# Performance work log

Hardware: AMD Instinct MI355X
Metric: run time of the kernel (lower is better)

## Reference

```python
import jax, jax.numpy as jnp
import numpy as np

B, S, D, H = 2, 2048, 1024, 16
DK = D // H

def setup_inputs() -> dict:
    key = jax.random.key(0)
    ks = jax.random.split(key, 5)
    scale = 1.0 / np.sqrt(D)
    return {
        "query": jax.random.normal(ks[0], (B, S, D), dtype=jnp.float32),
        "mask": jnp.ones((B, S, S), dtype=jnp.int32),
        "Wq": jax.random.normal(ks[1], (D, D), dtype=jnp.float32) * scale,
        "bq": jnp.zeros((D,), dtype=jnp.float32),
        "Wk": jax.random.normal(ks[2], (D, D), dtype=jnp.float32) * scale,
        "bk": jnp.zeros((D,), dtype=jnp.float32),
        "Wv": jax.random.normal(ks[3], (D, D), dtype=jnp.float32) * scale,
        "bv": jnp.zeros((D,), dtype=jnp.float32),
        "Wo": jax.random.normal(ks[4], (D, D), dtype=jnp.float32) * scale,
        "bo": jnp.zeros((D,), dtype=jnp.float32),
    }

def reference(query, mask, Wq, bq, Wk, bk, Wv, bv, Wo, bo):
    # self-attention: key = value = query (torch Linear: x @ W.T + b)
    b, s, d = query.shape
    def proj(x, W, bias):
        y = jnp.einsum('bsd,ed->bse', x, W) + bias
        return y.reshape(b, s, H, DK).transpose(0, 2, 1, 3)  # [B,H,S,DK]
    q = proj(query, Wq, bq)
    k = proj(query, Wk, bk)
    v = proj(query, Wv, bv)
    scores = jnp.einsum('bhqd,bhkd->bhqk', q, k) / jnp.sqrt(jnp.float32(DK))
    m = mask[:, None, :, :]  # [B,1,S,S] (torch unsqueeze(1) for 3D mask)
    scores = jnp.where(m == 0, jnp.float32(-1e9), scores)
    w = jax.nn.softmax(scores, axis=-1)  # dropout: eval mode -> identity
    o = jnp.einsum('bhqk,bhkd->bhqd', w, v)
    o = o.transpose(0, 2, 1, 3).reshape(b, s, d)
    return jnp.einsum('bsd,ed->bse', o, Wo) + bo
```

## Files before the change

### kernel.cpp

```cpp
#include <hip/hip_runtime.h>


typedef _Float16 f16x8 __attribute__((ext_vector_type(8)));
typedef _Float16 f16x4 __attribute__((ext_vector_type(4)));
typedef float    f32x4 __attribute__((ext_vector_type(4)));
typedef float    f32x16 __attribute__((ext_vector_type(16)));
typedef int      i32x4 __attribute__((ext_vector_type(4)));

#define MFMA32(a, b, c) __builtin_amdgcn_mfma_f32_32x32x16_f16(a, b, c, 0, 0, 0)
#define MFMA16(a, b, c) __builtin_amdgcn_mfma_f32_16x16x32_f16(a, b, c, 0, 0, 0)

__device__ __forceinline__ void gld16(const void* g, void* l) {
    __builtin_amdgcn_global_load_lds(
        (const __attribute__((address_space(1))) void*)g,
        (__attribute__((address_space(3))) void*)l, 16, 0, 0);
}

__device__ __forceinline__ void conv1k(const float* __restrict__ in,
                                       _Float16* __restrict__ out, int base) {
    const int i = base + threadIdx.x * 4;
    float4 v = *(const float4*)(in + i);
    f16x4 o;
    o.x = (_Float16)v.x; o.y = (_Float16)v.y; o.z = (_Float16)v.z; o.w = (_Float16)v.w;
    *(f16x4*)(out + i) = o;
}

__global__ void k_pre(const float* __restrict__ X, const float* __restrict__ Wq,
                      const float* __restrict__ Wk, const float* __restrict__ Wv,
                      const float* __restrict__ Wo,
                      _Float16* __restrict__ Xh, _Float16* __restrict__ Wqh,
                      _Float16* __restrict__ Wkh, _Float16* __restrict__ Wvh,
                      _Float16* __restrict__ Woh,
                      const int* __restrict__ mask, int* __restrict__ flag) {
    const int bid = blockIdx.x;
    if (bid < 4096)      conv1k(X,  Xh,  bid * 1024);
    else if (bid < 5120) conv1k(Wq, Wqh, (bid - 4096) * 1024);
    else if (bid < 6144) conv1k(Wk, Wkh, (bid - 5120) * 1024);
    else if (bid < 7168) conv1k(Wv, Wvh, (bid - 6144) * 1024);
    else if (bid < 8192) conv1k(Wo, Woh, (bid - 7168) * 1024);
    else {
        const int i = (bid - 8192) * 1024 + threadIdx.x * 4;
        int4 v = *(const int4*)(mask + i);
        if ((v.x == 0) | (v.y == 0) | (v.z == 0) | (v.w == 0)) atomicOr(flag, 1);
    }
}

__global__ __launch_bounds__(256, 3) void k_qkv(
    const _Float16* __restrict__ X,
    const _Float16* __restrict__ Wqh, const _Float16* __restrict__ Wkh,
    const _Float16* __restrict__ Wvh,
    const float* __restrict__ bq, const float* __restrict__ bk,
    const float* __restrict__ bv,
    _Float16* __restrict__ Qo, _Float16* __restrict__ Ko, _Float16* __restrict__ Vo)
{
    __shared__ _Float16 SH[128 * 136];
    _Float16* As = SH;
    _Float16* Bs = SH + 128 * 64;
    const int tid = threadIdx.x;
    const int lane = tid & 63, wv = tid >> 6;
    const int wrow = wv >> 1, wcol = wv & 1;
    const int l5 = lane & 31, half = lane >> 5;
    const int which = blockIdx.x >> 3;
    const _Float16* W   = which == 0 ? Wqh : which == 1 ? Wkh : Wvh;
    const float*   bias = which == 0 ? bq  : which == 1 ? bk  : bv;
    const int n0 = (blockIdx.x & 7) * 128;
    const int m0 = blockIdx.y * 128;

    f32x16 acc[2][2];
#pragma unroll
    for (int a = 0; a < 2; ++a)
#pragma unroll
        for (int bb = 0; bb < 2; ++bb)
#pragma unroll
            for (int r = 0; r < 16; ++r) acc[a][bb][r] = 0.f;

#pragma unroll 1
    for (int k0 = 0; k0 < 1024; k0 += 64) {
        __syncthreads();
#pragma unroll
        for (int it = 0; it < 4; ++it) {
            const int wbase = it * 256 + wv * 64;
            const int ci = wbase + lane;
            const int r = ci >> 3;
            const int c8 = (((ci & 7) ^ (r & 7)) * 8);
            gld16(X + (size_t)(m0 + r) * 1024 + k0 + c8, As + wbase * 8);
            gld16(W + (size_t)(n0 + r) * 1024 + k0 + c8, Bs + wbase * 8);
        }
        __syncthreads();
#pragma unroll
        for (int ks = 0; ks < 4; ++ks) {
            f16x8 af[2], bf[2];
#pragma unroll
            for (int mt = 0; mt < 2; ++mt)
                af[mt] = *(const f16x8*)(As + (wrow * 64 + mt * 32 + l5) * 64 +
                                         (((ks * 2 + half) ^ (l5 & 7)) * 8));
#pragma unroll
            for (int nt = 0; nt < 2; ++nt)
                bf[nt] = *(const f16x8*)(Bs + (wcol * 64 + nt * 32 + l5) * 64 +
                                         (((ks * 2 + half) ^ (l5 & 7)) * 8));
#pragma unroll
            for (int mt = 0; mt < 2; ++mt)
#pragma unroll
                for (int nt = 0; nt < 2; ++nt)
                    acc[mt][nt] = MFMA32(af[mt], bf[nt], acc[mt][nt]);
        }
    }

    __syncthreads();
    const int b_ = m0 >> 11;
    const int s_base = m0 & 2047;
    if (which == 2) {
#pragma unroll
        for (int nt = 0; nt < 2; ++nt) {
            const int e_l = wcol * 64 + nt * 32 + l5;
            const float bv_ = bias[n0 + e_l];
#pragma unroll
            for (int mt = 0; mt < 2; ++mt)
#pragma unroll
                for (int g = 0; g < 4; ++g) {
                    const int m_l = wrow * 64 + mt * 32 + 8 * g + 4 * half;
                    f16x4 pk;
#pragma unroll
                    for (int j = 0; j < 4; ++j)
                        pk[j] = (_Float16)(acc[mt][nt][4 * g + j] + bv_);
                    *(f16x4*)(SH + e_l * 136 + m_l) = pk;
                }
        }
        __syncthreads();
#pragma unroll
        for (int p = 0; p < 8; ++p) {
            const int e_l = p * 16 + (tid >> 4);
            const int s8 = (tid & 15) * 8;
            f16x8 vv = *(const f16x8*)(SH + e_l * 136 + s8);
            const int e = n0 + e_l;
            const int h = e >> 6, dk = e & 63;
            const int s0 = s_base + s8;
            const size_t idx = ((((size_t)(b_ * 16 + h) * 128 + (s0 >> 4)) * 2 +
                                (dk >> 5)) * 64 + (dk & 31) + 32 * ((s8 >> 3) & 1)) * 8;
            *(f16x8*)(Vo + idx) = vv;
        }
    } else {
        const float qs = (which == 0) ? 0.18033688011112042f : 1.0f;
#pragma unroll
        for (int nt = 0; nt < 2; ++nt) {
            const int e_l = wcol * 64 + nt * 32 + l5;
            const float bv_ = bias[n0 + e_l];
#pragma unroll
            for (int mt = 0; mt < 2; ++mt)
#pragma unroll
                for (int r = 0; r < 16; ++r) {
                    const int m_l = wrow * 64 + mt * 32 + (r & 3) + 8 * (r >> 2) + 4 * half;
                    SH[m_l * 136 + e_l] = (_Float16)((acc[mt][nt][r] + bv_) * qs);
                }
        }
        __syncthreads();
#pragma unroll
        for (int p = 0; p < 8; ++p) {
            const int m_l = p * 16 + (tid >> 4);
            const int c8 = (tid & 15) * 8;
            f16x8 vv = *(const f16x8*)(SH + m_l * 136 + c8);
            const int e = n0 + c8;
            const int h = e >> 6, dk = e & 63;
            const int s = s_base + m_l;
            if (which == 0) {
                *(f16x8*)(Qo + (((size_t)b_ * 16 + h) * 2048 + s) * 64 + dk) = vv;
            } else {
                const size_t idx = ((((size_t)(b_ * 16 + h) * 64 + (s >> 5)) * 4 +
                                    (dk >> 4)) * 64 + (s & 31) + 32 * ((dk >> 3) & 1)) * 8;
                *(f16x8*)(Ko + idx) = vv;
            }
        }
    }
}

__global__ __launch_bounds__(256, 4) void k_oproj(
    const _Float16* __restrict__ Oin, const _Float16* __restrict__ Woh,
    const float* __restrict__ bo, float* __restrict__ out)
{
    __shared__ _Float16 As[128 * 64];
    __shared__ _Float16 Bs[64 * 64];
    const int tid = threadIdx.x;
    const int lane = tid & 63, wv = tid >> 6;
    const int quad = lane >> 4, lc = lane & 15;
    const int n0 = blockIdx.x * 64;
    const int m0 = blockIdx.y * 128;

    const f32x4 fzero = {0.f, 0.f, 0.f, 0.f};
    f32x4 acc[2][4];
#pragma unroll
    for (int a = 0; a < 2; ++a)
#pragma unroll
        for (int bb = 0; bb < 4; ++bb) acc[a][bb] = fzero;

#pragma unroll 1
    for (int k0 = 0; k0 < 1024; k0 += 64) {
        __syncthreads();
#pragma unroll
        for (int it = 0; it < 4; ++it) {
            const int ci = it * 256 + tid;
            const int r = ci >> 3;
            const int c8 = (((ci & 7) ^ (r & 7)) * 8);
            gld16(Oin + (size_t)(m0 + r) * 1024 + k0 + c8, As + ci * 8);
        }
#pragma unroll
        for (int it = 0; it < 2; ++it) {
            const int ci = it * 256 + tid;
            const int r = ci >> 3;
            const int c8 = (((ci & 7) ^ (r & 7)) * 8);
            gld16(Woh + (size_t)(n0 + r) * 1024 + k0 + c8, Bs + ci * 8);
        }
        __syncthreads();
#pragma unroll
        for (int ks = 0; ks < 2; ++ks) {
            f16x8 af[2], bf[4];
#pragma unroll
            for (int mt = 0; mt < 2; ++mt)
                af[mt] = *(const f16x8*)(As + (wv * 32 + mt * 16 + lc) * 64 +
                                         (((ks * 4 + quad) ^ (lc & 7)) * 8));
#pragma unroll
            for (int nt = 0; nt < 4; ++nt)
                bf[nt] = *(const f16x8*)(Bs + (nt * 16 + lc) * 64 +
                                         (((ks * 4 + quad) ^ (lc & 7)) * 8));
#pragma unroll
            for (int mt = 0; mt < 2; ++mt)
#pragma unroll
                for (int nt = 0; nt < 4; ++nt)
                    acc[mt][nt] = MFMA16(af[mt], bf[nt], acc[mt][nt]);
        }
    }
#pragma unroll
    for (int nt = 0; nt < 4; ++nt) {
        const int e = n0 + nt * 16 + lc;
        const float bv_ = bo[e];
#pragma unroll
        for (int mt = 0; mt < 2; ++mt)
#pragma unroll
            for (int i = 0; i < 4; ++i) {
                const int m = m0 + wv * 32 + mt * 16 + quad * 4 + i;
                out[(size_t)m * 1024 + e] = acc[mt][nt][i] + bv_;
            }
    }
}

__global__ __launch_bounds__(256, 4) void k_attn(
    const _Float16* __restrict__ Q, const _Float16* __restrict__ Kp,
    const _Float16* __restrict__ Vp, const int* __restrict__ mask,
    const int* __restrict__ flag, _Float16* __restrict__ O)
{
    __shared__ float Os[2][32 * 64];
    __shared__ float Ls[2][32];

    const int tid = threadIdx.x;
    const int lane = tid & 63, wv = tid >> 6;
    const int l5 = lane & 31, half = lane >> 5;
    const int qt = wv >> 1, kh = wv & 1;
    const int bh = blockIdx.y;
    const int b = bh >> 4, h = bh & 15;
    const int qb = blockIdx.x * 64 + qt * 32;

    const _Float16* Qb = Q  + (size_t)bh * 2048 * 64;
    const _Float16* Kb = Kp + (size_t)bh * 131072;
    const _Float16* Vb = Vp + (size_t)bh * 131072;

    f16x8 qf[4];
#pragma unroll
    for (int kk = 0; kk < 4; ++kk)
        qf[kk] = *(const f16x8*)(Qb + (size_t)(qb + l5) * 64 + kk * 16 + half * 8);

    f32x16 o[2];
#pragma unroll
    for (int nt = 0; nt < 2; ++nt)
#pragma unroll
        for (int r = 0; r < 16; ++r) o[nt][r] = 0.f;
    float l_i = 0.f;

    const bool has_zero = (*flag != 0);

#pragma unroll 2
    for (int it = 0; it < 32; ++it) {
        const int kb = kh * 32 + it;
        f16x8 kf[4];
#pragma unroll
        for (int kk = 0; kk < 4; ++kk)
            kf[kk] = *(const f16x8*)(Kb + ((size_t)(kb * 4 + kk) * 64 + lane) * 8);
        f16x8 vf[4];
#pragma unroll
        for (int ks = 0; ks < 2; ++ks)
#pragma unroll
            for (int nt = 0; nt < 2; ++nt)
                vf[ks * 2 + nt] = *(const f16x8*)(Vb +
                    ((size_t)((kb * 2 + ks) * 2 + nt) * 64 + lane) * 8);

        f32x16 st;
#pragma unroll
        for (int r = 0; r < 16; ++r) st[r] = 0.f;
#pragma unroll
        for (int kk = 0; kk < 4; ++kk) st = MFMA32(kf[kk], qf[kk], st);

        if (has_zero) {
            const int q = qb + l5;
            const int* mr = mask + ((size_t)b * 2048 + q) * 2048 + kb * 32;
            for (int r = 0; r < 16; ++r) {
                const int kk_ = (r & 3) + 8 * (r >> 2) + 4 * half;
                if (mr[kk_] == 0) st[r] = -1e30f;
            }
        }

        float rs = 0.f;
#pragma unroll
        for (int r = 0; r < 16; ++r) {
            const float p = exp2f(st[r]);
            st[r] = p;
            rs += p;
        }
        rs += __shfl_xor(rs, 32);
        l_i += rs;

        int u[8], s[8];
#pragma unroll
        for (int j = 0; j < 8; ++j)
            u[j] = __builtin_bit_cast(int,
                       __builtin_amdgcn_cvt_pkrtz(st[2 * j], st[2 * j + 1]));
#pragma unroll
        for (int j = 0; j < 8; ++j) s[j] = __shfl_xor(u[j], 32);
        i32x4 a0 = { half ? s[2] : u[0], half ? s[3] : u[1],
                     half ? u[2] : s[0], half ? u[3] : s[1] };
        i32x4 a1 = { half ? s[6] : u[4], half ? s[7] : u[5],
                     half ? u[6] : s[4], half ? u[7] : s[5] };
        f16x8 pa0 = __builtin_bit_cast(f16x8, a0);
        f16x8 pa1 = __builtin_bit_cast(f16x8, a1);

        o[0] = MFMA32(pa0, vf[0], o[0]);
        o[1] = MFMA32(pa0, vf[1], o[1]);
        o[0] = MFMA32(pa1, vf[2], o[0]);
        o[1] = MFMA32(pa1, vf[3], o[1]);
    }

    if (kh == 1) {
        if (half == 0) Ls[qt][l5] = l_i;
#pragma unroll
        for (int nt = 0; nt < 2; ++nt)
#pragma unroll
            for (int r = 0; r < 16; ++r) {
                const int q_loc = (r & 3) + 8 * (r >> 2) + 4 * half;
                Os[qt][q_loc * 64 + nt * 32 + l5] = o[nt][r];
            }
    }
    __syncthreads();
    if (kh == 0) {
        const float linv = 1.f / (l_i + Ls[qt][l5]);
#pragma unroll
        for (int r = 0; r < 16; ++r) {
            const int q_loc = (r & 3) + 8 * (r >> 2) + 4 * half;
            const float lv = __shfl(linv, q_loc);
            const int q = qb + q_loc;
            _Float16* orow = O + ((size_t)b * 2048 + q) * 1024 + h * 64;
#pragma unroll
            for (int nt = 0; nt < 2; ++nt) {
                const float val = o[nt][r] + Os[qt][q_loc * 64 + nt * 32 + l5];
                orow[nt * 32 + l5] = (_Float16)(val * lv);
            }
        }
    }
}

extern "C" void kernel_launch(void* const* d_in, const int* in_sizes, int n_in,
                              void* d_out, int out_size, void* d_ws, size_t ws_size,
                              hipStream_t stream) {
    const float* query = (const float*)d_in[0];
    const int*   mask  = (const int*)d_in[1];
    const float* Wq = (const float*)d_in[2]; const float* bq = (const float*)d_in[3];
    const float* Wk = (const float*)d_in[4]; const float* bk = (const float*)d_in[5];
    const float* Wv = (const float*)d_in[6]; const float* bv = (const float*)d_in[7];
    const float* Wo = (const float*)d_in[8]; const float* bo = (const float*)d_in[9];
    float* out = (float*)d_out;

    char* ws = (char*)d_ws;
    _Float16* Xh  = (_Float16*)(ws);
    _Float16* Wqh = (_Float16*)(ws + 8388608);
    _Float16* Wkh = (_Float16*)(ws + 10485760);
    _Float16* Wvh = (_Float16*)(ws + 12582912);
    _Float16* Woh = (_Float16*)(ws + 14680064);
    _Float16* Qh  = (_Float16*)(ws + 16777216);
    _Float16* Kh  = (_Float16*)(ws + 25165824);
    _Float16* Vh  = (_Float16*)(ws + 33554432);
    _Float16* Oh  = Xh;
    int* flag     = (int*)(ws + 41943040);

    (void)hipMemsetAsync(flag, 0, 4, stream);
    k_pre<<<16384, 256, 0, stream>>>(query, Wq, Wk, Wv, Wo,
                                     Xh, Wqh, Wkh, Wvh, Woh, mask, flag);
    k_qkv<<<dim3(24, 32), 256, 0, stream>>>(Xh, Wqh, Wkh, Wvh, bq, bk, bv, Qh, Kh, Vh);
    k_attn<<<dim3(32, 32), 256, 0, stream>>>(Qh, Kh, Vh, mask, flag, Oh);
    k_oproj<<<dim3(16, 32), 256, 0, stream>>>(Oh, Woh, bo, out);
}
```

Baseline: 227.2 us.

## Split attention KV range four ways per query tile and use permlane32 swap

Each block now handles one 32-query tile with four waves that each cover a quarter of the key range, replacing two query tiles with a two-way key split. The grid doubles and launch bounds request higher occupancy, with a smaller shared reduction buffer that combines the partial outputs and row sums in two passes. The P-matrix lane exchange now uses permlane32_swap instead of shuffles and selects. The aim is more parallelism and less shuffle overhead, at the cost of more cross-wave reduction work, extra barriers, and Q fragments loaded once per 32 queries instead of per 64.

```diff
diff --git a/kernel.cpp b/kernel.cpp
--- a/kernel.cpp
+++ b/kernel.cpp
@@ -6,6 +6,7 @@
 typedef float    f32x4 __attribute__((ext_vector_type(4)));
 typedef float    f32x16 __attribute__((ext_vector_type(16)));
 typedef int      i32x4 __attribute__((ext_vector_type(4)));
+typedef unsigned u32x2 __attribute__((ext_vector_type(2)));
 
 #define MFMA32(a, b, c) __builtin_amdgcn_mfma_f32_32x32x16_f16(a, b, c, 0, 0, 0)
 #define MFMA16(a, b, c) __builtin_amdgcn_mfma_f32_16x16x32_f16(a, b, c, 0, 0, 0)
@@ -242,21 +243,20 @@
     }
 }
 
-__global__ __launch_bounds__(256, 4) void k_attn(
+__global__ __launch_bounds__(256, 8) void k_attn(
     const _Float16* __restrict__ Q, const _Float16* __restrict__ Kp,
     const _Float16* __restrict__ Vp, const int* __restrict__ mask,
     const int* __restrict__ flag, _Float16* __restrict__ O)
 {
-    __shared__ float Os[2][32 * 64];
-    __shared__ float Ls[2][32];
+    __shared__ float Os[3][32 * 32];
+    __shared__ float Ls[3][32];
 
     const int tid = threadIdx.x;
-    const int lane = tid & 63, wv = tid >> 6;
+    const int lane = tid & 63, kq = tid >> 6;
     const int l5 = lane & 31, half = lane >> 5;
-    const int qt = wv >> 1, kh = wv & 1;
     const int bh = blockIdx.y;
     const int b = bh >> 4, h = bh & 15;
-    const int qb = blockIdx.x * 64 + qt * 32;
+    const int qb = blockIdx.x * 32;
 
     const _Float16* Qb = Q  + (size_t)bh * 2048 * 64;
     const _Float16* Kb = Kp + (size_t)bh * 131072;
@@ -277,8 +277,8 @@
     const bool has_zero = (*flag != 0);
 
 #pragma unroll 2
-    for (int it = 0; it < 32; ++it) {
-        const int kb = kh * 32 + it;
+    for (int it = 0; it < 16; ++it) {
+        const int kb = kq * 16 + it;
         f16x8 kf[4];
 #pragma unroll
         for (int kk = 0; kk < 4; ++kk)
@@ -316,17 +316,17 @@
         rs += __shfl_xor(rs, 32);
         l_i += rs;
 
-        int u[8], s[8];
+        unsigned u[8];
 #pragma unroll
         for (int j = 0; j < 8; ++j)
-            u[j] = __builtin_bit_cast(int,
+            u[j] = __builtin_bit_cast(unsigned,
                        __builtin_amdgcn_cvt_pkrtz(st[2 * j], st[2 * j + 1]));
-#pragma unroll
-        for (int j = 0; j < 8; ++j) s[j] = __shfl_xor(u[j], 32);
-        i32x4 a0 = { half ? s[2] : u[0], half ? s[3] : u[1],
-                     half ? u[2] : s[0], half ? u[3] : s[1] };
-        i32x4 a1 = { half ? s[6] : u[4], half ? s[7] : u[5],
-                     half ? u[6] : s[4], half ? u[7] : s[5] };
+        u32x2 r02 = __builtin_amdgcn_permlane32_swap(u[0], u[2], false, false);
+        u32x2 r13 = __builtin_amdgcn_permlane32_swap(u[1], u[3], false, false);
+        u32x2 r46 = __builtin_amdgcn_permlane32_swap(u[4], u[6], false, false);
+        u32x2 r57 = __builtin_amdgcn_permlane32_swap(u[5], u[7], false, false);
+        i32x4 a0 = { (int)r02[0], (int)r13[0], (int)r02[1], (int)r13[1] };
+        i32x4 a1 = { (int)r46[0], (int)r57[0], (int)r46[1], (int)r57[1] };
         f16x8 pa0 = __builtin_bit_cast(f16x8, a0);
         f16x8 pa1 = __builtin_bit_cast(f16x8, a1);
 
@@ -336,30 +336,46 @@
         o[1] = MFMA32(pa1, vf[3], o[1]);
     }
 
-    if (kh == 1) {
-        if (half == 0) Ls[qt][l5] = l_i;
-#pragma unroll
-        for (int nt = 0; nt < 2; ++nt)
-#pragma unroll
-            for (int r = 0; r < 16; ++r) {
-                const int q_loc = (r & 3) + 8 * (r >> 2) + 4 * half;
-                Os[qt][q_loc * 64 + nt * 32 + l5] = o[nt][r];
-            }
+    if (kq != 0) {
+        if (half == 0) Ls[kq - 1][l5] = l_i;
+#pragma unroll
+        for (int r = 0; r < 16; ++r) {
+            const int q_loc = (r & 3) + 8 * (r >> 2) + 4 * half;
+            Os[kq - 1][q_loc * 32 + l5] = o[0][r];
+        }
     }
     __syncthreads();
-    if (kh == 0) {
-        const float linv = 1.f / (l_i + Ls[qt][l5]);
+    float linv = 0.f;
+    if (kq == 0) {
+        linv = 1.f / (l_i + Ls[0][l5] + Ls[1][l5] + Ls[2][l5]);
 #pragma unroll
         for (int r = 0; r < 16; ++r) {
             const int q_loc = (r & 3) + 8 * (r >> 2) + 4 * half;
             const float lv = __shfl(linv, q_loc);
             const int q = qb + q_loc;
-            _Float16* orow = O + ((size_t)b * 2048 + q) * 1024 + h * 64;
-#pragma unroll
-            for (int nt = 0; nt < 2; ++nt) {
-                const float val = o[nt][r] + Os[qt][q_loc * 64 + nt * 32 + l5];
-                orow[nt * 32 + l5] = (_Float16)(val * lv);
-            }
+            const float val = o[0][r] + Os[0][q_loc * 32 + l5] +
+                              Os[1][q_loc * 32 + l5] + Os[2][q_loc * 32 + l5];
+            O[((size_t)b * 2048 + q) * 1024 + h * 64 + l5] = (_Float16)(val * lv);
+        }
+    }
+    __syncthreads();
+    if (kq != 0) {
+#pragma unroll
+        for (int r = 0; r < 16; ++r) {
+            const int q_loc = (r & 3) + 8 * (r >> 2) + 4 * half;
+            Os[kq - 1][q_loc * 32 + l5] = o[1][r];
+        }
+    }
+    __syncthreads();
+    if (kq == 0) {
+#pragma unroll
+        for (int r = 0; r < 16; ++r) {
+            const int q_loc = (r & 3) + 8 * (r >> 2) + 4 * half;
+            const float lv = __shfl(linv, q_loc);
+            const int q = qb + q_loc;
+            const float val = o[1][r] + Os[0][q_loc * 32 + l5] +
+                              Os[1][q_loc * 32 + l5] + Os[2][q_loc * 32 + l5];
+            O[((size_t)b * 2048 + q) * 1024 + h * 64 + 32 + l5] = (_Float16)(val * lv);
         }
     }
 }
@@ -391,6 +407,6 @@
     k_pre<<<16384, 256, 0, stream>>>(query, Wq, Wk, Wv, Wo,
                                      Xh, Wqh, Wkh, Wvh, Woh, mask, flag);
     k_qkv<<<dim3(24, 32), 256, 0, stream>>>(Xh, Wqh, Wkh, Wvh, bq, bk, bv, Qh, Kh, Vh);
-    k_attn<<<dim3(32, 32), 256, 0, stream>>>(Qh, Kh, Vh, mask, flag, Oh);
+    k_attn<<<dim3(64, 32), 256, 0, stream>>>(Qh, Kh, Vh, mask, flag, Oh);
     k_oproj<<<dim3(16, 32), 256, 0, stream>>>(Oh, Woh, bo, out);
 }
```

New measurement: 706.9 us. +211.1%, slower.
